# Kernel tuning notes

Hardware: AMD Instinct MI355X
Metric: run time of the kernel (lower is better)

## Reference

```python
import jax, jax.numpy as jnp
import numpy as np

DIM = 1024
DEPTH = 8
DIM_HEAD = 64
HEADS = 16
NUM_Q = 16
EMB = 768
OUT = 1024
FF_INNER = 4 * DIM
INNER = DIM_HEAD * HEADS  # 1024
B, N1 = 64, 577
EPS = 1e-5


def _ln(x, g, b):
    mu = jnp.mean(x, axis=-1, keepdims=True)
    var = jnp.mean((x - mu) ** 2, axis=-1, keepdims=True)
    return (x - mu) * jax.lax.rsqrt(var + EPS) * g + b


def setup_inputs() -> dict:
    key = jax.random.key(0)
    ks = jax.random.split(key, 16)
    std = 0.02
    inp = {
        'x': jax.random.normal(ks[0], (B, N1, EMB), jnp.float32),
        'queries': jax.random.normal(ks[1], (1, NUM_Q, DIM), jnp.float32) / DIM ** 0.5,
        'proj_in_w': jax.random.normal(ks[2], (EMB, DIM), jnp.float32) * std,
        'proj_in_b': jnp.zeros((DIM,), jnp.float32),
        'ln1_g': jnp.ones((DEPTH, DIM), jnp.float32),
        'ln1_b': jnp.zeros((DEPTH, DIM), jnp.float32),
        'ln2_g': jnp.ones((DEPTH, DIM), jnp.float32),
        'ln2_b': jnp.zeros((DEPTH, DIM), jnp.float32),
        'wq': jax.random.normal(ks[3], (DEPTH, DIM, INNER), jnp.float32) * std,
        'wkv': jax.random.normal(ks[4], (DEPTH, DIM, 2 * INNER), jnp.float32) * std,
        'wo': jax.random.normal(ks[5], (DEPTH, INNER, DIM), jnp.float32) * std,
        'ffln_g': jnp.ones((DEPTH, DIM), jnp.float32),
        'ffln_b': jnp.zeros((DEPTH, DIM), jnp.float32),
        'w1': jax.random.normal(ks[6], (DEPTH, DIM, FF_INNER), jnp.float32) * std,
        'w2': jax.random.normal(ks[7], (DEPTH, FF_INNER, DIM), jnp.float32) * std,
        'proj_out_w': jax.random.normal(ks[8], (DIM, OUT), jnp.float32) * std,
        'proj_out_b': jnp.zeros((OUT,), jnp.float32),
        'nout_g': jnp.ones((OUT,), jnp.float32),
        'nout_b': jnp.zeros((OUT,), jnp.float32),
    }
    return inp


def reference(x, queries, proj_in_w, proj_in_b, ln1_g, ln1_b, ln2_g, ln2_b,
              wq, wkv, wo, ffln_g, ffln_b, w1, w2,
              proj_out_w, proj_out_b, nout_g, nout_b):
    b = x.shape[0]
    xp = x @ proj_in_w + proj_in_b          # (b, n1, dim)
    latents0 = jnp.broadcast_to(queries, (b, NUM_Q, DIM))
    scale = DIM_HEAD ** -0.25               # applied to both q and k

    def layer(latents, p):
        (g1, b1, g2, b2, Wq, Wkv, Wo, gf, bf, W1, W2) = p
        xn = _ln(xp, g1, b1)                # (b, n1, dim)
        lt = _ln(latents, g2, b2)           # (b, nq, dim)
        q = lt @ Wq                         # (b, nq, inner)
        kv_in = jnp.concatenate([xn, lt], axis=1)   # (b, n1+nq, dim)
        kv = kv_in @ Wkv                    # (b, n1+nq, 2*inner)
        k, v = jnp.split(kv, 2, axis=-1)
        L = kv_in.shape[1]
        qh = q.reshape(b, NUM_Q, HEADS, DIM_HEAD).transpose(0, 2, 1, 3)
        kh = k.reshape(b, L, HEADS, DIM_HEAD).transpose(0, 2, 1, 3)
        vh = v.reshape(b, L, HEADS, DIM_HEAD).transpose(0, 2, 1, 3)
        logits = jnp.einsum('bhqd,bhkd->bhqk', qh * scale, kh * scale)
        w = jax.nn.softmax(logits.astype(jnp.float32), axis=-1).astype(logits.dtype)
        o = jnp.einsum('bhqk,bhkd->bhqd', w, vh)
        o = o.transpose(0, 2, 1, 3).reshape(b, NUM_Q, INNER) @ Wo
        latents = o + latents
        h = _ln(latents, gf, bf) @ W1
        h = jax.nn.gelu(h, approximate=False)
        latents = h @ W2 + latents
        return latents, None

    params = (ln1_g, ln1_b, ln2_g, ln2_b, wq, wkv, wo, ffln_g, ffln_b, w1, w2)
    latents, _ = jax.lax.scan(layer, latents0, params)
    out = latents @ proj_out_w + proj_out_b
    return _ln(out, nout_g, nout_b)
```

## Files before the change

### kernel.cpp

```cpp
#include <hip/hip_runtime.h>
#include <hip/hip_bf16.h>
#include <math.h>

#define DEV __device__ __forceinline__

typedef __bf16 bf16x8 __attribute__((ext_vector_type(8)));
typedef float f32x4 __attribute__((ext_vector_type(4)));
typedef unsigned short u16x8 __attribute__((ext_vector_type(8)));
typedef unsigned short u16x4 __attribute__((ext_vector_type(4)));

DEV float b2f(unsigned short u){ unsigned int i = ((unsigned int)u)<<16; float f; __builtin_memcpy(&f,&i,4); return f; }
DEV unsigned short f2b(float x){ unsigned int i; __builtin_memcpy(&i,&x,4); unsigned int r = i + 0x7FFFu + ((i>>16)&1u); return (unsigned short)(r>>16); }

DEV int swz(int row, int elem){ return row*64 + ((((elem>>3) ^ row) & 7)<<3) + (elem&7); }

DEV int xcd_swz(int orig, int nwg){
  int q = nwg >> 3, r = nwg & 7;
  int x = orig & 7, idx = orig >> 3;
  return (x < r ? x*(q+1) : r*(q+1) + (x-r)*q) + idx;
}

enum { EPI_F32=0, EPI_GELU=2, EPI_RESF32=3 };

__global__ __launch_bounds__(512)
void gemm3(const unsigned short* __restrict__ A, const unsigned short* __restrict__ Bt,
           const float* __restrict__ bias, unsigned short* __restrict__ Out,
           int M, int N, int K, int NT)
{
    __shared__ unsigned short As[2][256*64];
    __shared__ unsigned short Bs[2][256*64];
    const int tid  = threadIdx.x;
    const int lane = tid & 63;
    const int wave = tid >> 6;
    const int wr = wave >> 2, wc = wave & 3;
    const int nb = xcd_swz(blockIdx.x, gridDim.x);
    const int nt = nb % NT, mt = nb / NT;
    const int lr = lane >> 3;
    const int lc = lane & 7;

    f32x4 acc[8][4];
    #pragma unroll
    for (int m=0;m<8;m++)
      #pragma unroll
      for (int n=0;n<4;n++) acc[m][n] = f32x4{0.f,0.f,0.f,0.f};

    const unsigned short* pA[4]; const unsigned short* pB[4];
    #pragma unroll
    for (int i=0;i<4;i++){
      int s = wave*4 + i;
      int row = s*8 + lr;
      int col = ((lc ^ row)&7)<<3;
      int gr = mt*256 + row; if (gr > M-1) gr = M-1;
      pA[i] = A + (size_t)gr*K + col;
      pB[i] = Bt + (size_t)(nt*256+row)*K + col;
    }

    auto stage = [&](int buf, int k0){
      #pragma unroll
      for (int i=0;i<4;i++){
        int s = wave*4 + i;
        __builtin_amdgcn_global_load_lds((const unsigned int*)(pA[i]+k0), (unsigned int*)&As[buf][s*512], 16, 0, 0);
      }
      #pragma unroll
      for (int i=0;i<4;i++){
        int s = wave*4 + i;
        __builtin_amdgcn_global_load_lds((const unsigned int*)(pB[i]+k0), (unsigned int*)&Bs[buf][s*512], 16, 0, 0);
      }
    };

    stage(0, 0);
    asm volatile("s_waitcnt vmcnt(0)" ::: "memory");
    __builtin_amdgcn_s_barrier();

    const int nk = K / 64;
    #pragma unroll 1
    for (int kt=0; kt<nk; kt++){
      const int cur = kt & 1;
      if (kt+1 < nk) stage(cur^1, (kt+1)*64);
      __builtin_amdgcn_sched_barrier(0);
      __builtin_amdgcn_s_setprio(1);
      #pragma unroll
      for (int kk=0; kk<2; kk++){
        bf16x8 bv[4];
        #pragma unroll
        for (int n=0;n<4;n++){
          int r = wc*64 + n*16 + (lane&15);
          bv[n] = (bf16x8)(*reinterpret_cast<const u16x8*>(&Bs[cur][swz(r, kk*32 + (lane>>4)*8)]));
        }
        #pragma unroll
        for (int m=0;m<8;m++){
          int r = wr*128 + m*16 + (lane&15);
          bf16x8 av = (bf16x8)(*reinterpret_cast<const u16x8*>(&As[cur][swz(r, kk*32 + (lane>>4)*8)]));
          #pragma unroll
          for (int n=0;n<4;n++)
            acc[m][n] = __builtin_amdgcn_mfma_f32_16x16x32_bf16(av, bv[n], acc[m][n], 0, 0, 0);
        }
      }
      __builtin_amdgcn_s_setprio(0);
      asm volatile("s_waitcnt vmcnt(0)" ::: "memory");
      __builtin_amdgcn_s_barrier();
    }

    #pragma unroll
    for (int m=0;m<8;m++){
      #pragma unroll
      for (int n=0;n<4;n++){
        #pragma unroll
        for (int r=0;r<4;r++){
          int row = mt*256 + wr*128 + m*16 + (lane>>4)*4 + r;
          int col = nt*256 + wc*64 + n*16 + (lane&15);
          if (row < M){
            float v = acc[m][n][r];
            if (bias) v += bias[col];
            Out[(size_t)row*N + col] = f2b(v);
          }
        }
      }
    }
}

template<int EPI>
__global__ __launch_bounds__(256)
void gemm_sp2(const unsigned short* __restrict__ AH, const unsigned short* __restrict__ AL,
              const unsigned short* __restrict__ BH, const unsigned short* __restrict__ BL,
              const float* __restrict__ bias, const float* __restrict__ Res,
              void* __restrict__ Out, unsigned short* __restrict__ OutL,
              int M, int N, int K, int NT)
{
    constexpr int MR=2, NR=2;
    __shared__ unsigned short As[2*64*64];
    __shared__ unsigned short Bs[2*64*64];
    const int tid  = threadIdx.x;
    const int lane = tid & 63;
    const int wave = tid >> 6;
    const int wr = wave >> 1, wc = wave & 1;
    const int chunk = gridDim.x >> 3;
    const int nb = (blockIdx.x & 7)*chunk + (blockIdx.x >> 3);
    const int nt = nb % NT, mt = nb / NT;

    f32x4 acc[MR][NR];
    #pragma unroll
    for (int m=0;m<MR;m++)
      #pragma unroll
      for (int n=0;n<NR;n++) acc[m][n] = f32x4{0.f,0.f,0.f,0.f};

    const unsigned short *pA[2], *pB[2];
    int dst[2];
    #pragma unroll
    for (int i=0;i<2;i++){
      int e = (i*256+tid)*8; int row = e>>6, col = e&63;
      pA[i] = AH + (size_t)(mt*64+row)*K + col;
      pB[i] = BH + (size_t)(nt*64+row)*K + col;
      dst[i] = swz(row,col);
    }
    const size_t dAL = (size_t)(AL - AH);
    const size_t dBL = (size_t)(BL - BH);

    u16x8 rAH0[2], rAL0[2], rBH0[2], rBL0[2];
    u16x8 rAH1[2], rAL1[2], rBH1[2], rBL1[2];
    auto issue0 = [&](int k0){
      #pragma unroll
      for (int i=0;i<2;i++){
        rAH0[i] = *reinterpret_cast<const u16x8*>(pA[i]+k0);
        rAL0[i] = *reinterpret_cast<const u16x8*>(pA[i]+dAL+k0);
        rBH0[i] = *reinterpret_cast<const u16x8*>(pB[i]+k0);
        rBL0[i] = *reinterpret_cast<const u16x8*>(pB[i]+dBL+k0);
      }
    };
    auto issue1 = [&](int k0){
      #pragma unroll
      for (int i=0;i<2;i++){
        rAH1[i] = *reinterpret_cast<const u16x8*>(pA[i]+k0);
        rAL1[i] = *reinterpret_cast<const u16x8*>(pA[i]+dAL+k0);
        rBH1[i] = *reinterpret_cast<const u16x8*>(pB[i]+k0);
        rBL1[i] = *reinterpret_cast<const u16x8*>(pB[i]+dBL+k0);
      }
    };
    auto commit0 = [&](){
      #pragma unroll
      for (int i=0;i<2;i++){
        *reinterpret_cast<u16x8*>(&As[dst[i]])      = rAH0[i];
        *reinterpret_cast<u16x8*>(&As[4096+dst[i]]) = rAL0[i];
        *reinterpret_cast<u16x8*>(&Bs[dst[i]])      = rBH0[i];
        *reinterpret_cast<u16x8*>(&Bs[4096+dst[i]]) = rBL0[i];
      }
    };
    auto commit1 = [&](){
      #pragma unroll
      for (int i=0;i<2;i++){
        *reinterpret_cast<u16x8*>(&As[dst[i]])      = rAH1[i];
        *reinterpret_cast<u16x8*>(&As[4096+dst[i]]) = rAL1[i];
        *reinterpret_cast<u16x8*>(&Bs[dst[i]])      = rBH1[i];
        *reinterpret_cast<u16x8*>(&Bs[4096+dst[i]]) = rBL1[i];
      }
    };
    auto compute = [&](){
      #pragma unroll
      for (int kk=0; kk<2; kk++){
        bf16x8 ah[MR], al[MR], bh[NR], bl[NR];
        #pragma unroll
        for (int m=0;m<MR;m++){
          int a = swz(wr*32 + m*16 + (lane&15), kk*32 + (lane>>4)*8);
          ah[m] = (bf16x8)(*reinterpret_cast<const u16x8*>(&As[a]));
          al[m] = (bf16x8)(*reinterpret_cast<const u16x8*>(&As[4096 + a]));
        }
        #pragma unroll
        for (int n=0;n<NR;n++){
          int a = swz(wc*32 + n*16 + (lane&15), kk*32 + (lane>>4)*8);
          bh[n] = (bf16x8)(*reinterpret_cast<const u16x8*>(&Bs[a]));
          bl[n] = (bf16x8)(*reinterpret_cast<const u16x8*>(&Bs[4096 + a]));
        }
        #pragma unroll
        for (int m=0;m<MR;m++)
          #pragma unroll
          for (int n=0;n<NR;n++){
            acc[m][n] = __builtin_amdgcn_mfma_f32_16x16x32_bf16(ah[m], bh[n], acc[m][n], 0, 0, 0);
            acc[m][n] = __builtin_amdgcn_mfma_f32_16x16x32_bf16(ah[m], bl[n], acc[m][n], 0, 0, 0);
            acc[m][n] = __builtin_amdgcn_mfma_f32_16x16x32_bf16(al[m], bh[n], acc[m][n], 0, 0, 0);
          }
      }
    };

    const int nk = K / 64;
    issue0(0); issue1(64);
    #pragma unroll 1
    for (int kt=0; kt<nk; kt+=2){
      __syncthreads();
      commit0();
      __syncthreads();
      if (kt+2 < nk) issue0((kt+2)*64);
      compute();
      __syncthreads();
      commit1();
      __syncthreads();
      if (kt+3 < nk) issue1((kt+3)*64);
      compute();
    }

    #pragma unroll
    for (int m=0;m<MR;m++){
      #pragma unroll
      for (int n=0;n<NR;n++){
        #pragma unroll
        for (int r=0;r<4;r++){
          int row = mt*64 + wr*32 + m*16 + (lane>>4)*4 + r;
          int col = nt*64 + wc*32 + n*16 + (lane&15);
          float v = acc[m][n][r];
          if (bias) v += bias[col];
          if constexpr (EPI==EPI_GELU){
            v = 0.5f*v*(1.0f + erff(v*0.70710678118654752f));
            unsigned short hi = f2b(v);
            ((unsigned short*)Out)[(size_t)row*N + col] = hi;
            OutL[(size_t)row*N + col] = f2b(v - b2f(hi));
          } else {
            if constexpr (EPI==EPI_RESF32) v += Res[(size_t)row*N + col];
            ((float*)Out)[(size_t)row*N + col] = v;
          }
        }
      }
    }
}

enum { OM_F32=0, OM_BF16=1, OM_SPLIT=2 };
template<bool INF32, int OM, bool HASGB>
__global__ __launch_bounds__(256)
void ln_rows(const void* __restrict__ In, void* __restrict__ Out,
             unsigned short* __restrict__ OutL,
             const float* __restrict__ g, const float* __restrict__ bb)
{
  const int row = blockIdx.x;
  const int tid = threadIdx.x;
  const size_t base = (size_t)row*1024 + tid*4;
  float v[4];
  if constexpr (INF32){
    f32x4 t = *reinterpret_cast<const f32x4*>((const float*)In + base);
    v[0]=t[0]; v[1]=t[1]; v[2]=t[2]; v[3]=t[3];
  } else {
    u16x4 t = *reinterpret_cast<const u16x4*>((const unsigned short*)In + base);
    #pragma unroll
    for (int j=0;j<4;j++) v[j] = b2f(t[j]);
  }
  float s = v[0]+v[1]+v[2]+v[3];
  float q = v[0]*v[0]+v[1]*v[1]+v[2]*v[2]+v[3]*v[3];
  #pragma unroll
  for (int o=32;o>0;o>>=1){ s += __shfl_xor(s,o,64); q += __shfl_xor(q,o,64); }
  __shared__ float sm[8];
  const int wave = tid>>6, lane = tid&63;
  if (lane==0){ sm[wave] = s; sm[4+wave] = q; }
  __syncthreads();
  s = sm[0]+sm[1]+sm[2]+sm[3];
  q = sm[4]+sm[5]+sm[6]+sm[7];
  const float mean = s*(1.f/1024.f);
  const float rstd = rsqrtf(fmaxf(q*(1.f/1024.f) - mean*mean, 0.f) + 1e-5f);
  #pragma unroll
  for (int j=0;j<4;j++){
    float t2 = (v[j]-mean)*rstd;
    if constexpr (HASGB) t2 = t2*g[tid*4+j] + bb[tid*4+j];
    v[j] = t2;
  }
  if constexpr (OM==OM_F32){
    f32x4 t{v[0],v[1],v[2],v[3]};
    *reinterpret_cast<f32x4*>((float*)Out + base) = t;
  } else if constexpr (OM==OM_BF16){
    u16x4 t{f2b(v[0]),f2b(v[1]),f2b(v[2]),f2b(v[3])};
    *reinterpret_cast<u16x4*>((unsigned short*)Out + base) = t;
  } else {
    u16x4 h{f2b(v[0]),f2b(v[1]),f2b(v[2]),f2b(v[3])};
    u16x4 l{f2b(v[0]-b2f(h[0])),f2b(v[1]-b2f(h[1])),f2b(v[2]-b2f(h[2])),f2b(v[3]-b2f(h[3]))};
    *reinterpret_cast<u16x4*>((unsigned short*)Out + base) = h;
    *reinterpret_cast<u16x4*>(OutL + base) = l;
  }
}

template<bool LO>
__global__ __launch_bounds__(256)
void transpose_cvt_b(const float* __restrict__ W, const float* __restrict__ rs,
                     unsigned short* __restrict__ Wt, unsigned short* __restrict__ Wtlo,
                     int K, int N, size_t wLS, size_t tLS, int dstRowOff)
{
  const int l = blockIdx.z;
  const float* Wl = W + (size_t)l*wLS;
  __shared__ float t[32][33];
  const int tx = threadIdx.x & 31, ty = threadIdx.x >> 5;
  const int n0 = blockIdx.x*32, k0 = blockIdx.y*32;
  #pragma unroll
  for (int j=0;j<4;j++){
    int r = ty + j*8;
    float w = Wl[(size_t)(k0+r)*N + n0 + tx];
    if (rs) w *= rs[l*1024 + k0+r];
    t[r][tx] = w;
  }
  __syncthreads();
  #pragma unroll
  for (int j=0;j<4;j++){
    int r = ty + j*8;
    float w = t[tx][r];
    unsigned short hi = f2b(w);
    size_t di = (size_t)l*tLS + (size_t)(dstRowOff + n0 + r)*K + k0 + tx;
    Wt[di] = hi;
    if constexpr (LO) Wtlo[di] = f2b(w - b2f(hi));
  }
}

__global__ __launch_bounds__(256)
void biaskv_kernel(const float* __restrict__ ln1b, const float* __restrict__ wkv,
                   float* __restrict__ out)
{
  const int l = blockIdx.y;
  const int n = blockIdx.x*256 + threadIdx.x;
  const float* b1 = ln1b + l*1024;
  const float* W  = wkv + (size_t)l*1024*2048;
  float s = 0.f;
  for (int k=0;k<1024;k++) s += b1[k]*W[(size_t)k*2048 + n];
  out[l*2048 + n] = s;
}

__global__ __launch_bounds__(256)
void init_latents(const float* __restrict__ Q, float* __restrict__ L)
{
  size_t idx = ((size_t)blockIdx.x*256 + threadIdx.x)*4;
  int row = (int)(idx >> 10);
  int col = (int)(idx & 1023);
  f32x4 t = *reinterpret_cast<const f32x4*>(Q + (size_t)(row & 15)*1024 + col);
  *reinterpret_cast<f32x4*>(L + idx) = t;
}

__global__ __launch_bounds__(256)
void cvt_f32_bf16(const float* __restrict__ In, unsigned short* __restrict__ Out, size_t n4)
{
  size_t i = (size_t)blockIdx.x*256 + threadIdx.x;
  if (i >= n4) return;
  f32x4 t = *reinterpret_cast<const f32x4*>(In + i*4);
  u16x4 u{f2b(t[0]),f2b(t[1]),f2b(t[2]),f2b(t[3])};
  *reinterpret_cast<u16x4*>(Out + i*4) = u;
}

__global__ __launch_bounds__(256)
void cvt_f32b_pair(const float* __restrict__ In, unsigned short* __restrict__ Oh,
                   unsigned short* __restrict__ Ol)
{
  size_t idx = ((size_t)blockIdx.x*256 + threadIdx.x)*4;
  f32x4 t = *reinterpret_cast<const f32x4*>(In + idx);
  u16x4 h{f2b(t[0]),f2b(t[1]),f2b(t[2]),f2b(t[3])};
  u16x4 l{f2b(t[0]-b2f(h[0])),f2b(t[1]-b2f(h[1])),f2b(t[2]-b2f(h[2])),f2b(t[3]-b2f(h[3]))};
  *reinterpret_cast<u16x4*>(Oh + idx) = h;
  *reinterpret_cast<u16x4*>(Ol + idx) = l;
}

__global__ __launch_bounds__(256)
void attn_kernel(const float* __restrict__ QKVf,
                 const unsigned short* __restrict__ KVX,
                 unsigned short* __restrict__ ATTOh,
                 unsigned short* __restrict__ ATTOl)
{
  __shared__ float qs[16][64];
  __shared__ float ws[16][600];
  const int tid = threadIdx.x;
  const int bh = blockIdx.x;
  const int b = bh >> 4, h = bh & 15;

  {
    int idx = tid*4;
    int qi = idx >> 6, d = idx & 63;
    f32x4 t = *reinterpret_cast<const f32x4*>(QKVf + (size_t)(b*16+qi)*3072 + h*64 + d);
    #pragma unroll
    for (int j=0;j<4;j++) qs[qi][d+j] = 0.125f * t[j];
  }
  __syncthreads();

  for (int r = tid; r < 593; r += 256){
    float a[16];
    #pragma unroll
    for (int qi=0;qi<16;qi++) a[qi] = 0.f;
    if (r < 577){
      const unsigned short* krow = KVX + ((size_t)(b*577 + r)*2048 + h*64);
      #pragma unroll 4
      for (int d4=0; d4<16; d4++){
        u16x4 k4 = *reinterpret_cast<const u16x4*>(krow + d4*4);
        float kf0=b2f(k4[0]), kf1=b2f(k4[1]), kf2=b2f(k4[2]), kf3=b2f(k4[3]);
        #pragma unroll
        for (int qi=0;qi<16;qi++){
          f32x4 q4 = *reinterpret_cast<const f32x4*>(&qs[qi][d4*4]);
          a[qi] += q4[0]*kf0 + q4[1]*kf1 + q4[2]*kf2 + q4[3]*kf3;
        }
      }
    } else {
      const float* krow = QKVf + (size_t)(b*16 + (r-577))*3072 + 1024 + h*64;
      #pragma unroll 4
      for (int d4=0; d4<16; d4++){
        f32x4 k4 = *reinterpret_cast<const f32x4*>(krow + d4*4);
        #pragma unroll
        for (int qi=0;qi<16;qi++){
          f32x4 q4 = *reinterpret_cast<const f32x4*>(&qs[qi][d4*4]);
          a[qi] += q4[0]*k4[0] + q4[1]*k4[1] + q4[2]*k4[2] + q4[3]*k4[3];
        }
      }
    }
    #pragma unroll
    for (int qi=0;qi<16;qi++) ws[qi][r] = a[qi];
  }
  __syncthreads();

  const int wave = tid>>6, lane = tid&63;
  for (int qi = wave; qi < 16; qi += 4){
    float m = -1e30f;
    for (int r = lane; r < 593; r += 64) m = fmaxf(m, ws[qi][r]);
    #pragma unroll
    for (int o=32;o>0;o>>=1) m = fmaxf(m, __shfl_xor(m,o,64));
    float s = 0.f;
    for (int r = lane; r < 593; r += 64){ float e = expf(ws[qi][r]-m); ws[qi][r] = e; s += e; }
    #pragma unroll
    for (int o=32;o>0;o>>=1) s += __shfl_xor(s,o,64);
    float inv = 1.f/s;
    for (int r = lane; r < 593; r += 64) ws[qi][r] *= inv;
  }
  __syncthreads();

  const int d = tid & 63, qg = tid >> 6;
  float o0=0.f,o1=0.f,o2=0.f,o3=0.f;
  for (int rr=0; rr<576; rr+=4){
    f32x4 w0 = *reinterpret_cast<const f32x4*>(&ws[qg   ][rr]);
    f32x4 w1 = *reinterpret_cast<const f32x4*>(&ws[qg+4 ][rr]);
    f32x4 w2 = *reinterpret_cast<const f32x4*>(&ws[qg+8 ][rr]);
    f32x4 w3 = *reinterpret_cast<const f32x4*>(&ws[qg+12][rr]);
    #pragma unroll
    for (int j=0;j<4;j++){
      const unsigned short* vrow = KVX + ((size_t)(b*577 + rr + j)*2048 + 1024 + h*64);
      float v = b2f(vrow[d]);
      o0 += w0[j]*v; o1 += w1[j]*v; o2 += w2[j]*v; o3 += w3[j]*v;
    }
  }
  {
    float v = b2f(KVX[(size_t)(b*577 + 576)*2048 + 1024 + h*64 + d]);
    o0 += ws[qg][576]*v; o1 += ws[qg+4][576]*v; o2 += ws[qg+8][576]*v; o3 += ws[qg+12][576]*v;
  }
  for (int r=577; r<593; r++){
    float v = QKVf[(size_t)(b*16 + (r-577))*3072 + 2048 + h*64 + d];
    o0 += ws[qg][r]*v; o1 += ws[qg+4][r]*v; o2 += ws[qg+8][r]*v; o3 += ws[qg+12][r]*v;
  }
  float ov[4] = {o0,o1,o2,o3};
  #pragma unroll
  for (int j=0;j<4;j++){
    size_t idx = (size_t)(b*16+qg+4*j)*1024 + h*64 + d;
    unsigned short hi = f2b(ov[j]);
    ATTOh[idx] = hi;
    ATTOl[idx] = f2b(ov[j] - b2f(hi));
  }
}

extern "C" void kernel_launch(void* const* d_in, const int* in_sizes, int n_in,
                              void* d_out, int out_size, void* d_ws, size_t ws_size,
                              hipStream_t stream)
{
  const float* x    = (const float*)d_in[0];
  const float* qry  = (const float*)d_in[1];
  const float* piw  = (const float*)d_in[2];
  const float* pib  = (const float*)d_in[3];
  const float* ln1g = (const float*)d_in[4];
  const float* ln1b = (const float*)d_in[5];
  const float* ln2g = (const float*)d_in[6];
  const float* ln2b = (const float*)d_in[7];
  const float* wq   = (const float*)d_in[8];
  const float* wkv  = (const float*)d_in[9];
  const float* wo   = (const float*)d_in[10];
  const float* ffg  = (const float*)d_in[11];
  const float* ffb  = (const float*)d_in[12];
  const float* w1   = (const float*)d_in[13];
  const float* w2   = (const float*)d_in[14];
  const float* pow_ = (const float*)d_in[15];
  const float* pob  = (const float*)d_in[16];
  const float* ng   = (const float*)d_in[17];
  const float* nb   = (const float*)d_in[18];

  const int MROWS = 64*577;
  char* wsb = (char*)d_ws;
  size_t off = 0;
  auto alloc = [&](size_t bytes)->char*{
    char* p = wsb + off; off = (off + bytes + 255) & ~(size_t)255; return p;
  };
  unsigned short* XB     = (unsigned short*)alloc((size_t)36992*768*2);
  unsigned short* XP     = (unsigned short*)alloc((size_t)36992*1024*2);
  unsigned short* KVX    = (unsigned short*)alloc((size_t)36992*2048*2);
  unsigned short* WpiT   = (unsigned short*)alloc((size_t)1024*768*2);
  unsigned short* WkvTs  = (unsigned short*)alloc((size_t)8*2048*1024*2);
  unsigned short* WqkvT  = (unsigned short*)alloc((size_t)8*3072*1024*2);
  unsigned short* WqkvTl = (unsigned short*)alloc((size_t)8*3072*1024*2);
  unsigned short* WoT    = (unsigned short*)alloc((size_t)8*1024*1024*2);
  unsigned short* WoTl   = (unsigned short*)alloc((size_t)8*1024*1024*2);
  unsigned short* W1T    = (unsigned short*)alloc((size_t)4096*1024*2);
  unsigned short* W1Tl   = (unsigned short*)alloc((size_t)4096*1024*2);
  unsigned short* W2T    = (unsigned short*)alloc((size_t)1024*4096*2);
  unsigned short* W2Tl   = (unsigned short*)alloc((size_t)1024*4096*2);
  float*          BKV    = (float*)alloc((size_t)8*2048*4);
  unsigned short* LTh    = (unsigned short*)alloc((size_t)1024*1024*2);
  unsigned short* LTl    = (unsigned short*)alloc((size_t)1024*1024*2);
  float*          QKVf   = (float*)alloc((size_t)1024*3072*4);
  unsigned short* ATTOh  = (unsigned short*)alloc((size_t)1024*1024*2);
  unsigned short* ATTOl  = (unsigned short*)alloc((size_t)1024*1024*2);
  unsigned short* FFHh   = (unsigned short*)alloc((size_t)1024*4096*2);
  unsigned short* FFHl   = (unsigned short*)alloc((size_t)1024*4096*2);
  unsigned short* LATBh  = (unsigned short*)alloc((size_t)1024*1024*2);
  unsigned short* LATBl  = (unsigned short*)alloc((size_t)1024*1024*2);
  float*          LATF   = (float*)alloc((size_t)1024*1024*4);
  if (off > ws_size) return;

  dim3 blk(256);
  dim3 blk5(512);

  cvt_f32_bf16<<<dim3((36928*768/4 + 255)/256), blk, 0, stream>>>(x, XB, (size_t)36928*768/4);
  transpose_cvt_b<false><<<dim3(32,24,1), blk, 0, stream>>>(piw, nullptr, WpiT, nullptr, 768, 1024, 0, 0, 0);
  transpose_cvt_b<false><<<dim3(64,32,8), blk, 0, stream>>>(wkv, ln1g, WkvTs, nullptr, 1024, 2048, (size_t)1024*2048, (size_t)2048*1024, 0);
  transpose_cvt_b<true ><<<dim3(32,32,8), blk, 0, stream>>>(wq,  nullptr, WqkvT, WqkvTl, 1024, 1024, (size_t)1024*1024, (size_t)3072*1024, 0);
  transpose_cvt_b<true ><<<dim3(64,32,8), blk, 0, stream>>>(wkv, nullptr, WqkvT, WqkvTl, 1024, 2048, (size_t)1024*2048, (size_t)3072*1024, 1024);
  transpose_cvt_b<true ><<<dim3(32,32,8), blk, 0, stream>>>(wo,  nullptr, WoT, WoTl, 1024, 1024, (size_t)1024*1024, (size_t)1024*1024, 0);
  biaskv_kernel<<<dim3(8,8), blk, 0, stream>>>(ln1b, wkv, BKV);
  init_latents<<<dim3(1024), blk, 0, stream>>>(qry, LATF);

  gemm3<<<dim3(145*4), blk5, 0, stream>>>(XB, WpiT, pib, XP, MROWS, 1024, 768, 4);
  ln_rows<false,OM_BF16,false><<<dim3(MROWS), blk, 0, stream>>>(XP, XP, nullptr, nullptr, nullptr);

  for (int l=0; l<8; l++){
    transpose_cvt_b<true><<<dim3(128,32,1), blk, 0, stream>>>(w1 + (size_t)l*1024*4096, nullptr, W1T, W1Tl, 1024, 4096, 0, 0, 0);
    transpose_cvt_b<true><<<dim3(32,128,1), blk, 0, stream>>>(w2 + (size_t)l*4096*1024, nullptr, W2T, W2Tl, 4096, 1024, 0, 0, 0);

    ln_rows<true,OM_SPLIT,true><<<dim3(1024), blk, 0, stream>>>(LATF, LTh, LTl, ln2g + l*1024, ln2b + l*1024);
    gemm_sp2<EPI_F32><<<dim3(16*48), blk, 0, stream>>>(
        LTh, LTl, WqkvT + (size_t)l*3072*1024, WqkvTl + (size_t)l*3072*1024,
        nullptr, nullptr, QKVf, nullptr, 1024, 3072, 1024, 48);
    gemm3<<<dim3(145*8), blk5, 0, stream>>>(
        XP, WkvTs + (size_t)l*2048*1024, BKV + l*2048, KVX, MROWS, 2048, 1024, 8);
    attn_kernel<<<dim3(1024), blk, 0, stream>>>(QKVf, KVX, ATTOh, ATTOl);
    gemm_sp2<EPI_RESF32><<<dim3(16*16), blk, 0, stream>>>(
        ATTOh, ATTOl, WoT + (size_t)l*1024*1024, WoTl + (size_t)l*1024*1024,
        nullptr, LATF, LATF, nullptr, 1024, 1024, 1024, 16);
    ln_rows<true,OM_SPLIT,true><<<dim3(1024), blk, 0, stream>>>(LATF, LTh, LTl, ffg + l*1024, ffb + l*1024);
    gemm_sp2<EPI_GELU><<<dim3(16*64), blk, 0, stream>>>(
        LTh, LTl, W1T, W1Tl, nullptr, nullptr, FFHh, FFHl, 1024, 4096, 1024, 64);
    gemm_sp2<EPI_RESF32><<<dim3(16*16), blk, 0, stream>>>(
        FFHh, FFHl, W2T, W2Tl, nullptr, LATF, LATF, nullptr, 1024, 1024, 4096, 16);
  }

  transpose_cvt_b<true><<<dim3(32,32,1), blk, 0, stream>>>(pow_, nullptr, W1T, W1Tl, 1024, 1024, 0, 0, 0);
  cvt_f32b_pair<<<dim3(1024), blk, 0, stream>>>(LATF, LATBh, LATBl);
  gemm_sp2<EPI_F32><<<dim3(16*16), blk, 0, stream>>>(
      LATBh, LATBl, W1T, W1Tl, pob, nullptr, QKVf, nullptr, 1024, 1024, 1024, 16);
  ln_rows<true,OM_F32,true><<<dim3(1024), blk, 0, stream>>>(QKVf, d_out, nullptr, ng, nb);
}
```

Baseline: 5.241 ms.

## Deepen GEMM prefetch pipelines with direct-to-LDS loads and split-K the FF2 GEMM

The large bf16 GEMM now keeps two K-tiles in flight, waiting on a partial vmcnt instead of draining all loads each step. The split-precision GEMM drops its register-staged copy path and loads hi/lo tiles straight into a double-buffered, pre-swizzled LDS layout. The K=4096 FF2 projection is split four ways into fp32 partials, followed by a separate reduce kernel that adds them into the residual, so that only 256 blocks no longer underfill the GPU. The cost is twice the LDS per block, extra partial-sum traffic, an additional launch per layer, and reuse of the XB buffer as scratch.

New measurement: 5.308 ms. No clear change (+1.3%).

```diff
diff --git a/kernel.cpp b/kernel.cpp
--- a/kernel.cpp
+++ b/kernel.cpp
@@ -23,7 +23,7 @@
 enum { EPI_F32=0, EPI_GELU=2, EPI_RESF32=3 };
 
 __global__ __launch_bounds__(512)
-void gemm3(const unsigned short* __restrict__ A, const unsigned short* __restrict__ Bt,
+void gemm4(const unsigned short* __restrict__ A, const unsigned short* __restrict__ Bt,
            const float* __restrict__ bias, unsigned short* __restrict__ Out,
            int M, int N, int K, int NT)
 {
@@ -68,17 +68,15 @@
       }
     };
 
+    const int nk = K / 64;
     stage(0, 0);
-    asm volatile("s_waitcnt vmcnt(0)" ::: "memory");
-    __builtin_amdgcn_s_barrier();
-
-    const int nk = K / 64;
+    stage(1, 64);
     #pragma unroll 1
     for (int kt=0; kt<nk; kt++){
       const int cur = kt & 1;
-      if (kt+1 < nk) stage(cur^1, (kt+1)*64);
-      __builtin_amdgcn_sched_barrier(0);
-      __builtin_amdgcn_s_setprio(1);
+      asm volatile("s_waitcnt vmcnt(8)" ::: "memory");
+      __builtin_amdgcn_s_barrier();
+      __builtin_amdgcn_sched_barrier(0);
       #pragma unroll
       for (int kk=0; kk<2; kk++){
         bf16x8 bv[4];
@@ -96,9 +94,10 @@
             acc[m][n] = __builtin_amdgcn_mfma_f32_16x16x32_bf16(av, bv[n], acc[m][n], 0, 0, 0);
         }
       }
-      __builtin_amdgcn_s_setprio(0);
-      asm volatile("s_waitcnt vmcnt(0)" ::: "memory");
+      __builtin_amdgcn_sched_barrier(0);
       __builtin_amdgcn_s_barrier();
+      __builtin_amdgcn_sched_barrier(0);
+      if (kt+2 < nk) stage(cur, (kt+2)*64);
     }
 
     #pragma unroll
@@ -121,15 +120,15 @@
 
 template<int EPI>
 __global__ __launch_bounds__(256)
-void gemm_sp2(const unsigned short* __restrict__ AH, const unsigned short* __restrict__ AL,
+void gemm_sp3(const unsigned short* __restrict__ AH, const unsigned short* __restrict__ AL,
               const unsigned short* __restrict__ BH, const unsigned short* __restrict__ BL,
               const float* __restrict__ bias, const float* __restrict__ Res,
               void* __restrict__ Out, unsigned short* __restrict__ OutL,
               int M, int N, int K, int NT)
 {
     constexpr int MR=2, NR=2;
-    __shared__ unsigned short As[2*64*64];
-    __shared__ unsigned short Bs[2*64*64];
+    __shared__ unsigned short As[2][2][64*64];
+    __shared__ unsigned short Bs[2][2][64*64];
     const int tid  = threadIdx.x;
     const int lane = tid & 63;
     const int wave = tid >> 6;
@@ -137,6 +136,8 @@
     const int chunk = gridDim.x >> 3;
     const int nb = (blockIdx.x & 7)*chunk + (blockIdx.x >> 3);
     const int nt = nb % NT, mt = nb / NT;
+    const int lr = lane >> 3;
+    const int lc = lane & 7;
 
     f32x4 acc[MR][NR];
     #pragma unroll
@@ -145,70 +146,51 @@
       for (int n=0;n<NR;n++) acc[m][n] = f32x4{0.f,0.f,0.f,0.f};
 
     const unsigned short *pA[2], *pB[2];
-    int dst[2];
     #pragma unroll
     for (int i=0;i<2;i++){
-      int e = (i*256+tid)*8; int row = e>>6, col = e&63;
+      int s = wave*2 + i;
+      int row = s*8 + lr;
+      int col = ((lc ^ row)&7)<<3;
       pA[i] = AH + (size_t)(mt*64+row)*K + col;
       pB[i] = BH + (size_t)(nt*64+row)*K + col;
-      dst[i] = swz(row,col);
     }
     const size_t dAL = (size_t)(AL - AH);
     const size_t dBL = (size_t)(BL - BH);
 
-    u16x8 rAH0[2], rAL0[2], rBH0[2], rBL0[2];
-    u16x8 rAH1[2], rAL1[2], rBH1[2], rBL1[2];
-    auto issue0 = [&](int k0){
+    auto stage = [&](int buf, int k0){
       #pragma unroll
       for (int i=0;i<2;i++){
-        rAH0[i] = *reinterpret_cast<const u16x8*>(pA[i]+k0);
-        rAL0[i] = *reinterpret_cast<const u16x8*>(pA[i]+dAL+k0);
-        rBH0[i] = *reinterpret_cast<const u16x8*>(pB[i]+k0);
-        rBL0[i] = *reinterpret_cast<const u16x8*>(pB[i]+dBL+k0);
+        int s = wave*2 + i;
+        __builtin_amdgcn_global_load_lds((const unsigned int*)(pA[i]+k0),     (unsigned int*)&As[buf][0][s*512], 16, 0, 0);
+        __builtin_amdgcn_global_load_lds((const unsigned int*)(pA[i]+dAL+k0), (unsigned int*)&As[buf][1][s*512], 16, 0, 0);
+        __builtin_amdgcn_global_load_lds((const unsigned int*)(pB[i]+k0),     (unsigned int*)&Bs[buf][0][s*512], 16, 0, 0);
+        __builtin_amdgcn_global_load_lds((const unsigned int*)(pB[i]+dBL+k0), (unsigned int*)&Bs[buf][1][s*512], 16, 0, 0);
       }
     };
-    auto issue1 = [&](int k0){
-      #pragma unroll
-      for (int i=0;i<2;i++){
-        rAH1[i] = *reinterpret_cast<const u16x8*>(pA[i]+k0);
-        rAL1[i] = *reinterpret_cast<const u16x8*>(pA[i]+dAL+k0);
-        rBH1[i] = *reinterpret_cast<const u16x8*>(pB[i]+k0);
-        rBL1[i] = *reinterpret_cast<const u16x8*>(pB[i]+dBL+k0);
-      }
-    };
-    auto commit0 = [&](){
-      #pragma unroll
-      for (int i=0;i<2;i++){
-        *reinterpret_cast<u16x8*>(&As[dst[i]])      = rAH0[i];
-        *reinterpret_cast<u16x8*>(&As[4096+dst[i]]) = rAL0[i];
-        *reinterpret_cast<u16x8*>(&Bs[dst[i]])      = rBH0[i];
-        *reinterpret_cast<u16x8*>(&Bs[4096+dst[i]]) = rBL0[i];
-      }
-    };
-    auto commit1 = [&](){
-      #pragma unroll
-      for (int i=0;i<2;i++){
-        *reinterpret_cast<u16x8*>(&As[dst[i]])      = rAH1[i];
-        *reinterpret_cast<u16x8*>(&As[4096+dst[i]]) = rAL1[i];
-        *reinterpret_cast<u16x8*>(&Bs[dst[i]])      = rBH1[i];
-        *reinterpret_cast<u16x8*>(&Bs[4096+dst[i]]) = rBL1[i];
-      }
-    };
-    auto compute = [&](){
+
+    const int nk = K / 64;
+    stage(0, 0);
+    stage(1, 64);
+    #pragma unroll 1
+    for (int kt=0; kt<nk; kt++){
+      const int cur = kt & 1;
+      asm volatile("s_waitcnt vmcnt(8)" ::: "memory");
+      __builtin_amdgcn_s_barrier();
+      __builtin_amdgcn_sched_barrier(0);
       #pragma unroll
       for (int kk=0; kk<2; kk++){
         bf16x8 ah[MR], al[MR], bh[NR], bl[NR];
         #pragma unroll
         for (int m=0;m<MR;m++){
           int a = swz(wr*32 + m*16 + (lane&15), kk*32 + (lane>>4)*8);
-          ah[m] = (bf16x8)(*reinterpret_cast<const u16x8*>(&As[a]));
-          al[m] = (bf16x8)(*reinterpret_cast<const u16x8*>(&As[4096 + a]));
+          ah[m] = (bf16x8)(*reinterpret_cast<const u16x8*>(&As[cur][0][a]));
+          al[m] = (bf16x8)(*reinterpret_cast<const u16x8*>(&As[cur][1][a]));
         }
         #pragma unroll
         for (int n=0;n<NR;n++){
           int a = swz(wc*32 + n*16 + (lane&15), kk*32 + (lane>>4)*8);
-          bh[n] = (bf16x8)(*reinterpret_cast<const u16x8*>(&Bs[a]));
-          bl[n] = (bf16x8)(*reinterpret_cast<const u16x8*>(&Bs[4096 + a]));
+          bh[n] = (bf16x8)(*reinterpret_cast<const u16x8*>(&Bs[cur][0][a]));
+          bl[n] = (bf16x8)(*reinterpret_cast<const u16x8*>(&Bs[cur][1][a]));
         }
         #pragma unroll
         for (int m=0;m<MR;m++)
@@ -219,22 +201,10 @@
             acc[m][n] = __builtin_amdgcn_mfma_f32_16x16x32_bf16(al[m], bh[n], acc[m][n], 0, 0, 0);
           }
       }
-    };
-
-    const int nk = K / 64;
-    issue0(0); issue1(64);
-    #pragma unroll 1
-    for (int kt=0; kt<nk; kt+=2){
-      __syncthreads();
-      commit0();
-      __syncthreads();
-      if (kt+2 < nk) issue0((kt+2)*64);
-      compute();
-      __syncthreads();
-      commit1();
-      __syncthreads();
-      if (kt+3 < nk) issue1((kt+3)*64);
-      compute();
+      __builtin_amdgcn_sched_barrier(0);
+      __builtin_amdgcn_s_barrier();
+      __builtin_amdgcn_sched_barrier(0);
+      if (kt+2 < nk) stage(cur, (kt+2)*64);
     }
 
     #pragma unroll
@@ -259,6 +229,125 @@
         }
       }
     }
+}
+
+__global__ __launch_bounds__(256)
+void gemm_spk3(const unsigned short* __restrict__ AH, const unsigned short* __restrict__ AL,
+               const unsigned short* __restrict__ BH, const unsigned short* __restrict__ BL,
+               float* __restrict__ PART, int M, int N, int Kstride, int Klen, int NT)
+{
+    constexpr int MR=2, NR=2;
+    __shared__ unsigned short As[2][2][64*64];
+    __shared__ unsigned short Bs[2][2][64*64];
+    const int tid  = threadIdx.x;
+    const int lane = tid & 63;
+    const int wave = tid >> 6;
+    const int wr = wave >> 1, wc = wave & 1;
+    const int nblk = (M>>6)*(N>>6);
+    const int kchunk = blockIdx.x / nblk;
+    const int rem = blockIdx.x - kchunk*nblk;
+    const int cpx = nblk >> 3;
+    const int nb = (rem & 7)*cpx + (rem >> 3);
+    const int nt = nb % NT, mt = nb / NT;
+    const int kbase = kchunk*Klen;
+    const int lr = lane >> 3;
+    const int lc = lane & 7;
+
+    f32x4 acc[MR][NR];
+    #pragma unroll
+    for (int m=0;m<MR;m++)
+      #pragma unroll
+      for (int n=0;n<NR;n++) acc[m][n] = f32x4{0.f,0.f,0.f,0.f};
+
+    const unsigned short *pA[2], *pB[2];
+    #pragma unroll
+    for (int i=0;i<2;i++){
+      int s = wave*2 + i;
+      int row = s*8 + lr;
+      int col = ((lc ^ row)&7)<<3;
+      pA[i] = AH + (size_t)(mt*64+row)*Kstride + kbase + col;
+      pB[i] = BH + (size_t)(nt*64+row)*Kstride + kbase + col;
+    }
+    const size_t dAL = (size_t)(AL - AH);
+    const size_t dBL = (size_t)(BL - BH);
+
+    auto stage = [&](int buf, int k0){
+      #pragma unroll
+      for (int i=0;i<2;i++){
+        int s = wave*2 + i;
+        __builtin_amdgcn_global_load_lds((const unsigned int*)(pA[i]+k0),     (unsigned int*)&As[buf][0][s*512], 16, 0, 0);
+        __builtin_amdgcn_global_load_lds((const unsigned int*)(pA[i]+dAL+k0), (unsigned int*)&As[buf][1][s*512], 16, 0, 0);
+        __builtin_amdgcn_global_load_lds((const unsigned int*)(pB[i]+k0),     (unsigned int*)&Bs[buf][0][s*512], 16, 0, 0);
+        __builtin_amdgcn_global_load_lds((const unsigned int*)(pB[i]+dBL+k0), (unsigned int*)&Bs[buf][1][s*512], 16, 0, 0);
+      }
+    };
+
+    const int nk = Klen / 64;
+    stage(0, 0);
+    stage(1, 64);
+    #pragma unroll 1
+    for (int kt=0; kt<nk; kt++){
+      const int cur = kt & 1;
+      asm volatile("s_waitcnt vmcnt(8)" ::: "memory");
+      __builtin_amdgcn_s_barrier();
+      __builtin_amdgcn_sched_barrier(0);
+      #pragma unroll
+      for (int kk=0; kk<2; kk++){
+        bf16x8 ah[MR], al[MR], bh[NR], bl[NR];
+        #pragma unroll
+        for (int m=0;m<MR;m++){
+          int a = swz(wr*32 + m*16 + (lane&15), kk*32 + (lane>>4)*8);
+          ah[m] = (bf16x8)(*reinterpret_cast<const u16x8*>(&As[cur][0][a]));
+          al[m] = (bf16x8)(*reinterpret_cast<const u16x8*>(&As[cur][1][a]));
+        }
+        #pragma unroll
+        for (int n=0;n<NR;n++){
+          int a = swz(wc*32 + n*16 + (lane&15), kk*32 + (lane>>4)*8);
+          bh[n] = (bf16x8)(*reinterpret_cast<const u16x8*>(&Bs[cur][0][a]));
+          bl[n] = (bf16x8)(*reinterpret_cast<const u16x8*>(&Bs[cur][1][a]));
+        }
+        #pragma unroll
+        for (int m=0;m<MR;m++)
+          #pragma unroll
+          for (int n=0;n<NR;n++){
+            acc[m][n] = __builtin_amdgcn_mfma_f32_16x16x32_bf16(ah[m], bh[n], acc[m][n], 0, 0, 0);
+            acc[m][n] = __builtin_amdgcn_mfma_f32_16x16x32_bf16(ah[m], bl[n], acc[m][n], 0, 0, 0);
+            acc[m][n] = __builtin_amdgcn_mfma_f32_16x16x32_bf16(al[m], bh[n], acc[m][n], 0, 0, 0);
+          }
+      }
+      __builtin_amdgcn_sched_barrier(0);
+      __builtin_amdgcn_s_barrier();
+      __builtin_amdgcn_sched_barrier(0);
+      if (kt+2 < nk) stage(cur, (kt+2)*64);
+    }
+
+    float* out = PART + (size_t)kchunk*M*N;
+    #pragma unroll
+    for (int m=0;m<MR;m++){
+      #pragma unroll
+      for (int n=0;n<NR;n++){
+        #pragma unroll
+        for (int r=0;r<4;r++){
+          int row = mt*64 + wr*32 + m*16 + (lane>>4)*4 + r;
+          int col = nt*64 + wc*32 + n*16 + (lane&15);
+          out[(size_t)row*N + col] = acc[m][n][r];
+        }
+      }
+    }
+}
+
+__global__ __launch_bounds__(256)
+void reduce4_res(const float* __restrict__ PART, float* __restrict__ LATF)
+{
+  size_t i = ((size_t)blockIdx.x*256 + threadIdx.x)*4;
+  f32x4 a = *reinterpret_cast<const f32x4*>(PART + i);
+  f32x4 b = *reinterpret_cast<const f32x4*>(PART + 1048576 + i);
+  f32x4 c = *reinterpret_cast<const f32x4*>(PART + 2097152 + i);
+  f32x4 d = *reinterpret_cast<const f32x4*>(PART + 3145728 + i);
+  f32x4 r = *reinterpret_cast<f32x4*>(LATF + i);
+  #pragma unroll
+  for (int j=0;j<4;j++) r[j] += a[j]+b[j]+c[j]+d[j];
+  *reinterpret_cast<f32x4*>(LATF + i) = r;
 }
 
 enum { OM_F32=0, OM_BF16=1, OM_SPLIT=2 };
@@ -543,6 +632,7 @@
   unsigned short* LATBl  = (unsigned short*)alloc((size_t)1024*1024*2);
   float*          LATF   = (float*)alloc((size_t)1024*1024*4);
   if (off > ws_size) return;
+  float* PART = (float*)XB;
 
   dim3 blk(256);
   dim3 blk5(512);
@@ -556,7 +646,7 @@
   biaskv_kernel<<<dim3(8,8), blk, 0, stream>>>(ln1b, wkv, BKV);
   init_latents<<<dim3(1024), blk, 0, stream>>>(qry, LATF);
 
-  gemm3<<<dim3(145*4), blk5, 0, stream>>>(XB, WpiT, pib, XP, MROWS, 1024, 768, 4);
+  gemm4<<<dim3(145*4), blk5, 0, stream>>>(XB, WpiT, pib, XP, MROWS, 1024, 768, 4);
   ln_rows<false,OM_BF16,false><<<dim3(MROWS), blk, 0, stream>>>(XP, XP, nullptr, nullptr, nullptr);
 
   for (int l=0; l<8; l++){
@@ -564,25 +654,26 @@
     transpose_cvt_b<true><<<dim3(32,128,1), blk, 0, stream>>>(w2 + (size_t)l*4096*1024, nullptr, W2T, W2Tl, 4096, 1024, 0, 0, 0);
 
     ln_rows<true,OM_SPLIT,true><<<dim3(1024), blk, 0, stream>>>(LATF, LTh, LTl, ln2g + l*1024, ln2b + l*1024);
-    gemm_sp2<EPI_F32><<<dim3(16*48), blk, 0, stream>>>(
+    gemm_sp3<EPI_F32><<<dim3(16*48), blk, 0, stream>>>(
         LTh, LTl, WqkvT + (size_t)l*3072*1024, WqkvTl + (size_t)l*3072*1024,
         nullptr, nullptr, QKVf, nullptr, 1024, 3072, 1024, 48);
-    gemm3<<<dim3(145*8), blk5, 0, stream>>>(
+    gemm4<<<dim3(145*8), blk5, 0, stream>>>(
         XP, WkvTs + (size_t)l*2048*1024, BKV + l*2048, KVX, MROWS, 2048, 1024, 8);
     attn_kernel<<<dim3(1024), blk, 0, stream>>>(QKVf, KVX, ATTOh, ATTOl);
-    gemm_sp2<EPI_RESF32><<<dim3(16*16), blk, 0, stream>>>(
+    gemm_sp3<EPI_RESF32><<<dim3(16*16), blk, 0, stream>>>(
         ATTOh, ATTOl, WoT + (size_t)l*1024*1024, WoTl + (size_t)l*1024*1024,
         nullptr, LATF, LATF, nullptr, 1024, 1024, 1024, 16);
     ln_rows<true,OM_SPLIT,true><<<dim3(1024), blk, 0, stream>>>(LATF, LTh, LTl, ffg + l*1024, ffb + l*1024);
-    gemm_sp2<EPI_GELU><<<dim3(16*64), blk, 0, stream>>>(
+    gemm_sp3<EPI_GELU><<<dim3(16*64), blk, 0, stream>>>(
         LTh, LTl, W1T, W1Tl, nullptr, nullptr, FFHh, FFHl, 1024, 4096, 1024, 64);
-    gemm_sp2<EPI_RESF32><<<dim3(16*16), blk, 0, stream>>>(
-        FFHh, FFHl, W2T, W2Tl, nullptr, LATF, LATF, nullptr, 1024, 1024, 4096, 16);
+    gemm_spk3<<<dim3(4*16*16), blk, 0, stream>>>(
+        FFHh, FFHl, W2T, W2Tl, PART, 1024, 1024, 4096, 1024, 16);
+    reduce4_res<<<dim3(1024), blk, 0, stream>>>(PART, LATF);
   }
 
   transpose_cvt_b<true><<<dim3(32,32,1), blk, 0, stream>>>(pow_, nullptr, W1T, W1Tl, 1024, 1024, 0, 0, 0);
   cvt_f32b_pair<<<dim3(1024), blk, 0, stream>>>(LATF, LATBh, LATBl);
-  gemm_sp2<EPI_F32><<<dim3(16*16), blk, 0, stream>>>(
+  gemm_sp3<EPI_F32><<<dim3(16*16), blk, 0, stream>>>(
       LATBh, LATBl, W1T, W1Tl, pob, nullptr, QKVf, nullptr, 1024, 1024, 1024, 16);
   ln_rows<true,OM_F32,true><<<dim3(1024), blk, 0, stream>>>(QKVf, d_out, nullptr, ng, nb);
 }
```
